# Optimization experiments

Hardware: AMD Instinct MI355X
Metric: run time of the kernel (lower is better)

## Reference

```python
import jax, jax.numpy as jnp
import numpy as np
from jax import lax

N = 100000
IN_C, HID, OUT_C = 512, 256, 128
K_STEPS = 10
ALPHA = 0.1
RES_ALPHA = 1.0
LN_EPS = 1e-5


def layer_norm(h, g, b):
    mu = jnp.mean(h, axis=-1, keepdims=True)
    var = jnp.mean(jnp.square(h - mu), axis=-1, keepdims=True)
    return (h - mu) * lax.rsqrt(var + LN_EPS) * g + b


def appnp(h, src, dst):
    # add self loops
    loop = jnp.arange(N, dtype=src.dtype)
    s = jnp.concatenate([src, loop])
    d = jnp.concatenate([dst, loop])
    ew = jnp.ones(s.shape[0], h.dtype)
    deg = jax.ops.segment_sum(ew, d, num_segments=N)
    dis = jnp.where(deg > 0, lax.rsqrt(jnp.maximum(deg, 1e-12)), 0.0)
    norm = dis[s] * ew * dis[d]  # [E+N]
    h0 = h
    def step(carry, _):
        msg = norm[:, None] * carry[s]                      # gather [E+N, C]
        agg = jax.ops.segment_sum(msg, d, num_segments=N)    # scatter-add
        return (1.0 - ALPHA) * agg + ALPHA * h0, None
    h, _ = lax.scan(step, h, None, length=K_STEPS)
    return h


def setup_inputs() -> dict:
    key = jax.random.key(0)
    ks = jax.random.split(key, 12)
    def lin(k, fan_in, fan_out):
        bound = 1.0 / np.sqrt(fan_in)
        kw, kb = jax.random.split(k)
        W = jax.random.uniform(kw, (fan_in, fan_out), jnp.float32, -bound, bound)
        b = jax.random.uniform(kb, (fan_out,), jnp.float32, -bound, bound)
        return W, b
    x = jax.random.normal(ks[0], (N, IN_C), jnp.float32)
    edge_index = jax.random.randint(ks[1], (2, 1600000), 0, N, jnp.int32)
    W_in, b_in = lin(ks[2], IN_C, HID)
    W1, b1 = lin(ks[3], HID, HID)
    W2, b2 = lin(ks[4], HID, HID)
    W_out, b_out = lin(ks[5], HID, OUT_C)
    g1 = jnp.ones(HID); be1 = jnp.zeros(HID)
    g2 = jnp.ones(HID); be2 = jnp.zeros(HID)
    return {"x": x, "edge_index": edge_index,
            "W_in": W_in, "b_in": b_in,
            "W1": W1, "b1": b1, "g1": g1, "be1": be1,
            "W2": W2, "b2": b2, "g2": g2, "be2": be2,
            "W_out": W_out, "b_out": b_out}


def reference(x, edge_index, W_in, b_in, W1, b1, g1, be1, W2, b2, g2, be2, W_out, b_out):
    # MLP with residual blocks (eval mode: no dropout)
    h = x @ W_in + b_in
    for (W, b, g, be) in ((W1, b1, g1, be1), (W2, b2, g2, be2)):
        identity = h
        h = layer_norm(h @ W + b, g, be)
        h = RES_ALPHA * h + (1.0 - RES_ALPHA) * identity
        h = jax.nn.relu(h)
    h = h @ W_out + b_out
    # APPNP propagation
    return appnp(h, edge_index[0], edge_index[1])
```

## Files before the change

kernel.cpp:

```cpp
#include <hip/hip_runtime.h>

typedef unsigned short u16;
typedef __attribute__((ext_vector_type(8))) short bfrag;
typedef __attribute__((ext_vector_type(4))) float f32x4;

__device__ inline float b2f(u16 u) {
    union { unsigned int i; float f; } v; v.i = ((unsigned int)u) << 16; return v.f;
}
__device__ inline u16 f2b(float f) {
    union { float f; unsigned int u; } v; v.f = f;
    unsigned int r = v.u + 0x7fffu + ((v.u >> 16) & 1u);
    return (u16)(r >> 16);
}
__device__ inline float ldF(const void* p, size_t i, bool bf) {
    return bf ? b2f(((const u16*)p)[i]) : ((const float*)p)[i];
}
__device__ inline void gload_lds16(const void* g, void* l) {
    __builtin_amdgcn_global_load_lds((const __attribute__((address_space(1))) unsigned int*)g,
                                     (__attribute__((address_space(3))) unsigned int*)l, 16, 0, 0);
}

__global__ void detect_k(const unsigned int* __restrict__ g1w, int* flag) {
    if (blockIdx.x == 0 && threadIdx.x == 0)
        *flag = (g1w[0] == 0x3F803F80u) ? 1 : 0;
}

__global__ void cvt_x(const void* __restrict__ in, u16* __restrict__ out, int n4,
                      const int* __restrict__ flagp) {
    int i = blockIdx.x * 256 + threadIdx.x;
    if (i >= n4) return;
    if (*flagp) {
        ((ushort4*)out)[i] = ((const ushort4*)in)[i];
    } else {
        const float4 v = ((const float4*)in)[i];
        ushort4 o; o.x = f2b(v.x); o.y = f2b(v.y); o.z = f2b(v.z); o.w = f2b(v.w);
        ((ushort4*)out)[i] = o;
    }
}

__global__ void cvt_h0b(const float* __restrict__ h0, u16* __restrict__ out, int n64) {
    int i = blockIdx.x * 256 + threadIdx.x;
    if (i >= n64) return;
    const float2 v = ((const float2*)h0)[i];
    ((unsigned int*)out)[i] = ((unsigned int)f2b(v.y) << 16) | (unsigned int)f2b(v.x);
}

__global__ void wt_k(const void* __restrict__ W, u16* __restrict__ Wt, int K, int NC,
                     const int* __restrict__ flagp) {
    int i = blockIdx.x * 256 + threadIdx.x;
    if (i >= K * NC) return;
    int k = i / NC, nn = i - k * NC;
    u16 v = (*flagp) ? ((const u16*)W)[i] : f2b(((const float*)W)[i]);
    Wt[(size_t)nn * K + k] = v;
}

template<int K, bool OUT_BF16>
__global__ __launch_bounds__(256) void gemm_bt(const u16* __restrict__ A, const u16* __restrict__ Bt,
                                               const void* __restrict__ bias, void* __restrict__ C,
                                               int M, int NC, const int* __restrict__ flagp) {
    const int BM = 128, BN = 128, BK = 32;
    __shared__ u16 As[2][BM * BK];
    __shared__ u16 Bs[2][BN * BK];
    const bool bf = (*flagp != 0);
    int nt = NC / BN;

    int nwg = gridDim.x, bid = blockIdx.x;
    int qc = nwg >> 3, rc = nwg & 7;
    int xcd = bid & 7, off = bid >> 3;
    int swz = (xcd < rc ? xcd * (qc + 1) : rc * (qc + 1) + (xcd - rc) * qc) + off;
    int m0 = (swz / nt) * BM;
    int n0 = (swz % nt) * BN;

    int t = threadIdx.x;
    int lane = t & 63, wave = t >> 6;
    int wm = (wave >> 1) * 64, wn = (wave & 1) * 64;

    f32x4 acc[4][4];
#pragma unroll
    for (int i = 0; i < 4; i++)
#pragma unroll
        for (int j = 0; j < 4; j++) acc[i][j] = (f32x4){0.f, 0.f, 0.f, 0.f};

    auto stage = [&](int bufi, int kk) {
#pragma unroll
        for (int q = 0; q < 2; ++q) {
            int idx = q * 256 + t;
            int row = idx >> 2;
            int cb  = (idx & 3) * 16;
            int ra = m0 + row; ra = ra < M ? ra : M - 1;
            const char* ga = (const char*)A  + ((size_t)ra * K) * 2 + kk * 2 + cb;
            const char* gb = (const char*)Bt + ((size_t)(n0 + row) * K) * 2 + kk * 2 + cb;
            char* la = (char*)&As[bufi][0] + q * 4096 + wave * 1024;
            char* lb = (char*)&Bs[bufi][0] + q * 4096 + wave * 1024;
            gload_lds16(ga, la);
            gload_lds16(gb, lb);
        }
    };

    stage(0, 0);
    __syncthreads();
    int cur = 0;
    int r16 = lane & 15, q8 = (lane >> 4) * 8;
    for (int k0 = 0; k0 < K; k0 += BK) {
        if (k0 + BK < K) stage(cur ^ 1, k0 + BK);
        bfrag a[4], b[4];
#pragma unroll
        for (int i = 0; i < 4; i++) a[i] = *(const bfrag*)&As[cur][(wm + i * 16 + r16) * BK + q8];
#pragma unroll
        for (int j = 0; j < 4; j++) b[j] = *(const bfrag*)&Bs[cur][(wn + j * 16 + r16) * BK + q8];
#pragma unroll
        for (int i = 0; i < 4; i++)
#pragma unroll
            for (int j = 0; j < 4; j++)
                acc[i][j] = __builtin_amdgcn_mfma_f32_16x16x32_bf16(a[i], b[j], acc[i][j], 0, 0, 0);
        __syncthreads();
        cur ^= 1;
    }

    int q4 = (lane >> 4) * 4;
#pragma unroll
    for (int j = 0; j < 4; j++) {
        int cg = n0 + wn + j * 16 + r16;
        float bvv = ldF(bias, cg, bf);
#pragma unroll
        for (int i = 0; i < 4; i++) {
#pragma unroll
            for (int rr = 0; rr < 4; rr++) {
                int rg = m0 + wm + i * 16 + q4 + rr;
                if (rg < M) {
                    float v = acc[i][j][rr] + bvv;
                    if (OUT_BF16) ((u16*)C)[(size_t)rg * NC + cg] = f2b(v);
                    else          ((float*)C)[(size_t)rg * NC + cg] = v;
                }
            }
        }
    }
}

__global__ __launch_bounds__(256) void ln_relu_k(const float* __restrict__ T, const void* __restrict__ g,
                                                 const void* __restrict__ be, u16* __restrict__ out,
                                                 int M, const int* __restrict__ flagp) {
    const bool bf = (*flagp != 0);
    int wave = threadIdx.x >> 6, lane = threadIdx.x & 63;
    int row = blockIdx.x * 4 + wave;
    if (row >= M) return;
    const float4 x = *(const float4*)(T + (size_t)row * 256 + lane * 4);
    float s = x.x + x.y + x.z + x.w;
    for (int o = 32; o > 0; o >>= 1) s += __shfl_xor(s, o);
    float mu = s * (1.0f / 256.0f);
    float d0 = x.x - mu, d1 = x.y - mu, d2 = x.z - mu, d3 = x.w - mu;
    float q = d0 * d0 + d1 * d1 + d2 * d2 + d3 * d3;
    for (int o = 32; o > 0; o >>= 1) q += __shfl_xor(q, o);
    float rs = rsqrtf(q * (1.0f / 256.0f) + 1e-5f);
    int c0 = lane * 4;
    float y0 = fmaxf(d0 * rs * ldF(g, c0 + 0, bf) + ldF(be, c0 + 0, bf), 0.f);
    float y1 = fmaxf(d1 * rs * ldF(g, c0 + 1, bf) + ldF(be, c0 + 1, bf), 0.f);
    float y2 = fmaxf(d2 * rs * ldF(g, c0 + 2, bf) + ldF(be, c0 + 2, bf), 0.f);
    float y3 = fmaxf(d3 * rs * ldF(g, c0 + 3, bf) + ldF(be, c0 + 3, bf), 0.f);
    ushort4 o4; o4.x = f2b(y0); o4.y = f2b(y1); o4.z = f2b(y2); o4.w = f2b(y3);
    *(ushort4*)(out + (size_t)row * 256 + c0) = o4;
}

__global__ void deg_init(int* deg, int n) {
    int i = blockIdx.x * 256 + threadIdx.x;
    if (i < n) deg[i] = 1;
}
__global__ void deg_count(const int* __restrict__ dst, int* deg, int E) {
    int i = blockIdx.x * 256 + threadIdx.x;
    if (i < E) atomicAdd(&deg[dst[i]], 1);
}
__global__ void dis_k(const int* __restrict__ deg, float* dis, int n) {
    int i = blockIdx.x * 256 + threadIdx.x;
    if (i < n) dis[i] = rsqrtf((float)deg[i]);
}

__global__ void scan_block(const int* __restrict__ deg, int* rowptr, int* bsum, int n) {
    __shared__ int sh[256];
    int t = threadIdx.x, i = blockIdx.x * 256 + t;
    int v = (i < n) ? deg[i] : 0;
    sh[t] = v; __syncthreads();
    for (int o = 1; o < 256; o <<= 1) {
        int x = (t >= o) ? sh[t - o] : 0;
        __syncthreads();
        sh[t] += x;
        __syncthreads();
    }
    if (i < n) rowptr[i] = sh[t] - v;
    if (t == 255) bsum[blockIdx.x] = sh[t];
}
__global__ void scan_sums(int* bsum, int nb) {
    __shared__ int sh[512];
    int t = threadIdx.x;
    int v = (t < nb) ? bsum[t] : 0;
    sh[t] = v; __syncthreads();
    for (int o = 1; o < 512; o <<= 1) {
        int x = (t >= o) ? sh[t - o] : 0;
        __syncthreads();
        sh[t] += x;
        __syncthreads();
    }
    if (t < nb) bsum[t] = sh[t] - v;
}
__global__ void scan_add(int* rowptr, const int* __restrict__ bsum, int n, int total) {
    int i = blockIdx.x * 256 + threadIdx.x;
    if (i < n) rowptr[i] += bsum[blockIdx.x];
    if (i == 0) rowptr[n] = total;
}
__global__ void fill_k(const int* __restrict__ src, const int* __restrict__ dst,
                       const int* __restrict__ rowptr, int* cursor, const float* __restrict__ dis,
                       int* col, float* wt, int E, int n) {
    int i = blockIdx.x * 256 + threadIdx.x;
    if (i >= E + n) return;
    int s, d;
    if (i < E) { s = src[i]; d = dst[i]; }
    else       { s = d = i - E; }
    int p = rowptr[d] + atomicAdd(&cursor[d], 1);
    col[p] = s;
    wt[p] = dis[s] * dis[d];
}

__global__ __launch_bounds__(256) void prop_k(const u16* __restrict__ curb, const float* __restrict__ h0,
                                              const int* __restrict__ rowptr, const int* __restrict__ col,
                                              const float* __restrict__ wt,
                                              u16* __restrict__ outB, void* __restrict__ outD,
                                              const int* __restrict__ flagp, int n) {
    int wave = threadIdx.x >> 6, lane = threadIdx.x & 63;
    int node = blockIdx.x * 4 + wave;
    if (node >= n) return;
    int p0 = rowptr[node], p1 = rowptr[node + 1];
    float ax = 0.f, ay = 0.f;
    for (int p = p0; p < p1; p += 64) {
        int cnt = p1 - p; if (cnt > 64) cnt = 64;
        int sj = 0; float wj = 0.f;
        if (lane < cnt) { sj = col[p + lane]; wj = wt[p + lane]; }
        for (int j = 0; j < cnt; j += 8) {
            float ww[8]; unsigned int v[8];
#pragma unroll
            for (int u = 0; u < 8; ++u) {
                int jj = j + u;
                bool ok = jj < cnt;
                if (!ok) jj = cnt - 1;
                int ss = __shfl(sj, jj);
                float w = __shfl(wj, jj);
                ww[u] = ok ? w : 0.f;
                v[u] = *(const unsigned int*)(curb + (size_t)ss * 128 + 2 * lane);
            }
#pragma unroll
            for (int u = 0; u < 8; ++u) {
                ax = fmaf(ww[u], b2f((u16)(v[u] & 0xffffu)), ax);
                ay = fmaf(ww[u], b2f((u16)(v[u] >> 16)), ay);
            }
        }
    }
    const float2 h = *(const float2*)(h0 + (size_t)node * 128 + 2 * lane);
    float rx = 0.9f * ax + 0.1f * h.x;
    float ry = 0.9f * ay + 0.1f * h.y;
    if (outB) {
        unsigned int pk = ((unsigned int)f2b(ry) << 16) | (unsigned int)f2b(rx);
        ((unsigned int*)outB)[(size_t)node * 64 + lane] = pk;
    } else if (*flagp) {
        unsigned int pk = ((unsigned int)f2b(ry) << 16) | (unsigned int)f2b(rx);
        ((unsigned int*)outD)[(size_t)node * 64 + lane] = pk;
    } else {
        float2 o; o.x = rx; o.y = ry;
        *(float2*)((float*)outD + (size_t)node * 128 + 2 * lane) = o;
    }
}

extern "C" void kernel_launch(void* const* d_in, const int* in_sizes, int n_in,
                              void* d_out, int out_size, void* d_ws, size_t ws_size,
                              hipStream_t stream) {
    const int N = in_sizes[0] / 512;
    const int E = in_sizes[1] / 2;
    const void* x    = d_in[0];
    const int*  ei   = (const int*)d_in[1];
    const void* Win  = d_in[2];
    const void* bin  = d_in[3];
    const void* W1   = d_in[4];
    const void* b1   = d_in[5];
    const void* g1   = d_in[6];
    const void* be1  = d_in[7];
    const void* W2   = d_in[8];
    const void* b2   = d_in[9];
    const void* g2   = d_in[10];
    const void* be2  = d_in[11];
    const void* Wout = d_in[12];
    const void* bout = d_in[13];
    (void)n_in; (void)out_size; (void)ws_size;

    char* w = (char*)d_ws;
    auto alloc = [&](size_t b) { char* p = w; w += (b + 255) & ~(size_t)255; return p; };
    char*  buf0 = alloc((size_t)N * 512 * 2);
    char*  actAraw = alloc((size_t)N * 256 * 2);
    float* h0   = (float*)alloc((size_t)N * 128 * 4);
    u16* WtIn  = (u16*)alloc((size_t)512 * 256 * 2);
    u16* Wt1   = (u16*)alloc((size_t)256 * 256 * 2);
    u16* Wt2   = (u16*)alloc((size_t)256 * 256 * 2);
    u16* WtOut = (u16*)alloc((size_t)256 * 128 * 2);
    int*   deg    = (int*)alloc((size_t)N * 4);
    float* dis    = (float*)alloc((size_t)N * 4);
    int*   rowptr = (int*)alloc((size_t)(N + 1) * 4);
    int*   cursor = (int*)alloc((size_t)N * 4);
    int*   bsum   = (int*)alloc(512 * 4);
    int*   flag   = (int*)alloc(256);
    u16*   xbf = (u16*)buf0;
    float* T   = (float*)buf0;
    u16*   h0b = (u16*)buf0;
    u16*   cA  = (u16*)(buf0 + (size_t)N * 128 * 2);
    u16*   cB  = (u16*)(buf0 + (size_t)N * 128 * 4);
    u16*   actA = (u16*)actAraw;
    int*   ecol = (int*)actAraw;
    float* ewt  = (float*)(actAraw + (size_t)(E + N) * 4);

    detect_k<<<1, 64, 0, stream>>>((const unsigned int*)g1, flag);

    int n4 = N * 512 / 4;
    cvt_x<<<(n4 + 255) / 256, 256, 0, stream>>>(x, xbf, n4, flag);
    wt_k<<<(512 * 256 + 255) / 256, 256, 0, stream>>>(Win,  WtIn,  512, 256, flag);
    wt_k<<<(256 * 256 + 255) / 256, 256, 0, stream>>>(W1,   Wt1,   256, 256, flag);
    wt_k<<<(256 * 256 + 255) / 256, 256, 0, stream>>>(W2,   Wt2,   256, 256, flag);
    wt_k<<<(256 * 128 + 255) / 256, 256, 0, stream>>>(Wout, WtOut, 256, 128, flag);

    int mt = (N + 127) / 128;
    gemm_bt<512, true ><<<mt * 2, 256, 0, stream>>>(xbf,  WtIn,  bin,  actA, N, 256, flag);
    gemm_bt<256, false><<<mt * 2, 256, 0, stream>>>(actA, Wt1,   b1,   T,    N, 256, flag);
    ln_relu_k<<<(N + 3) / 4, 256, 0, stream>>>(T, g1, be1, actA, N, flag);
    gemm_bt<256, false><<<mt * 2, 256, 0, stream>>>(actA, Wt2,   b2,   T,    N, 256, flag);
    ln_relu_k<<<(N + 3) / 4, 256, 0, stream>>>(T, g2, be2, actA, N, flag);
    gemm_bt<256, false><<<mt * 1, 256, 0, stream>>>(actA, WtOut, bout, h0,   N, 128, flag);

    cvt_h0b<<<(N * 64 + 255) / 256, 256, 0, stream>>>(h0, h0b, N * 64);

    deg_init <<<(N + 255) / 256, 256, 0, stream>>>(deg, N);
    deg_count<<<(E + 255) / 256, 256, 0, stream>>>(ei + E, deg, E);
    dis_k    <<<(N + 255) / 256, 256, 0, stream>>>(deg, dis, N);
    int nb = (N + 255) / 256;
    scan_block<<<nb, 256, 0, stream>>>(deg, rowptr, bsum, N);
    scan_sums<<<1, 512, 0, stream>>>(bsum, nb);
    scan_add<<<nb, 256, 0, stream>>>(rowptr, bsum, N, E + N);
    hipMemsetAsync(cursor, 0, (size_t)N * 4, stream);
    fill_k<<<(E + N + 255) / 256, 256, 0, stream>>>(ei, ei + E, rowptr, cursor, dis, ecol, ewt, E, N);

    const u16* cur = h0b;
    for (int it = 0; it < 10; ++it) {
        bool last = (it == 9);
        u16* o = (it & 1) ? cB : cA;
        prop_k<<<(N + 3) / 4, 256, 0, stream>>>(cur, h0, rowptr, ecol, ewt,
                                                last ? nullptr : o,
                                                last ? d_out : nullptr, flag, N);
        cur = o;
    }
}
```

Baseline: 1.520 ms.

## Pack edge col/weight, store h0 in bf16, unroll gather by sixteen

Edge source index and weight are packed into one int2 array, so each edge costs one load instead of two. The output GEMM now writes h0 directly in bf16, which removes the fp32 h0 buffer and the separate conversion kernel, and each propagation step reads the bf16 copy for its residual term. The gather inner loop is unrolled to 16 outstanding loads to raise memory-level parallelism, and the degree init kernel is replaced by a memset with the self-loop +1 folded into later kernels. The bf16 residual adds rounding error to the alpha*h0 term, and the wider unroll raises register use.

```diff
diff --git a/kernel.cpp b/kernel.cpp
--- a/kernel.cpp
+++ b/kernel.cpp
@@ -36,13 +36,6 @@
         ushort4 o; o.x = f2b(v.x); o.y = f2b(v.y); o.z = f2b(v.z); o.w = f2b(v.w);
         ((ushort4*)out)[i] = o;
     }
-}
-
-__global__ void cvt_h0b(const float* __restrict__ h0, u16* __restrict__ out, int n64) {
-    int i = blockIdx.x * 256 + threadIdx.x;
-    if (i >= n64) return;
-    const float2 v = ((const float2*)h0)[i];
-    ((unsigned int*)out)[i] = ((unsigned int)f2b(v.y) << 16) | (unsigned int)f2b(v.x);
 }
 
 __global__ void wt_k(const void* __restrict__ W, u16* __restrict__ Wt, int K, int NC,
@@ -161,23 +154,19 @@
     *(ushort4*)(out + (size_t)row * 256 + c0) = o4;
 }
 
-__global__ void deg_init(int* deg, int n) {
-    int i = blockIdx.x * 256 + threadIdx.x;
-    if (i < n) deg[i] = 1;
-}
 __global__ void deg_count(const int* __restrict__ dst, int* deg, int E) {
     int i = blockIdx.x * 256 + threadIdx.x;
     if (i < E) atomicAdd(&deg[dst[i]], 1);
 }
 __global__ void dis_k(const int* __restrict__ deg, float* dis, int n) {
     int i = blockIdx.x * 256 + threadIdx.x;
-    if (i < n) dis[i] = rsqrtf((float)deg[i]);
+    if (i < n) dis[i] = rsqrtf((float)(deg[i] + 1));
 }
 
 __global__ void scan_block(const int* __restrict__ deg, int* rowptr, int* bsum, int n) {
     __shared__ int sh[256];
     int t = threadIdx.x, i = blockIdx.x * 256 + t;
-    int v = (i < n) ? deg[i] : 0;
+    int v = (i < n) ? deg[i] + 1 : 0;
     sh[t] = v; __syncthreads();
     for (int o = 1; o < 256; o <<= 1) {
         int x = (t >= o) ? sh[t - o] : 0;
@@ -208,20 +197,20 @@
 }
 __global__ void fill_k(const int* __restrict__ src, const int* __restrict__ dst,
                        const int* __restrict__ rowptr, int* cursor, const float* __restrict__ dis,
-                       int* col, float* wt, int E, int n) {
+                       int2* __restrict__ epack, int E, int n) {
     int i = blockIdx.x * 256 + threadIdx.x;
     if (i >= E + n) return;
     int s, d;
     if (i < E) { s = src[i]; d = dst[i]; }
     else       { s = d = i - E; }
     int p = rowptr[d] + atomicAdd(&cursor[d], 1);
-    col[p] = s;
-    wt[p] = dis[s] * dis[d];
-}
-
-__global__ __launch_bounds__(256) void prop_k(const u16* __restrict__ curb, const float* __restrict__ h0,
-                                              const int* __restrict__ rowptr, const int* __restrict__ col,
-                                              const float* __restrict__ wt,
+    float wv = dis[s] * dis[d];
+    int2 e; e.x = s; e.y = __float_as_int(wv);
+    epack[p] = e;
+}
+
+__global__ __launch_bounds__(256) void prop_k(const u16* __restrict__ curb, const u16* __restrict__ h0b,
+                                              const int* __restrict__ rowptr, const int2* __restrict__ epack,
                                               u16* __restrict__ outB, void* __restrict__ outD,
                                               const int* __restrict__ flagp, int n) {
     int wave = threadIdx.x >> 6, lane = threadIdx.x & 63;
@@ -232,11 +221,14 @@
     for (int p = p0; p < p1; p += 64) {
         int cnt = p1 - p; if (cnt > 64) cnt = 64;
         int sj = 0; float wj = 0.f;
-        if (lane < cnt) { sj = col[p + lane]; wj = wt[p + lane]; }
-        for (int j = 0; j < cnt; j += 8) {
-            float ww[8]; unsigned int v[8];
-#pragma unroll
-            for (int u = 0; u < 8; ++u) {
+        if (lane < cnt) {
+            int2 e = epack[p + lane];
+            sj = e.x; wj = __int_as_float(e.y);
+        }
+        for (int j = 0; j < cnt; j += 16) {
+            float ww[16]; unsigned int v[16];
+#pragma unroll
+            for (int u = 0; u < 16; ++u) {
                 int jj = j + u;
                 bool ok = jj < cnt;
                 if (!ok) jj = cnt - 1;
@@ -246,15 +238,15 @@
                 v[u] = *(const unsigned int*)(curb + (size_t)ss * 128 + 2 * lane);
             }
 #pragma unroll
-            for (int u = 0; u < 8; ++u) {
+            for (int u = 0; u < 16; ++u) {
                 ax = fmaf(ww[u], b2f((u16)(v[u] & 0xffffu)), ax);
                 ay = fmaf(ww[u], b2f((u16)(v[u] >> 16)), ay);
             }
         }
     }
-    const float2 h = *(const float2*)(h0 + (size_t)node * 128 + 2 * lane);
-    float rx = 0.9f * ax + 0.1f * h.x;
-    float ry = 0.9f * ay + 0.1f * h.y;
+    unsigned int hp = ((const unsigned int*)h0b)[(size_t)node * 64 + lane];
+    float rx = 0.9f * ax + 0.1f * b2f((u16)(hp & 0xffffu));
+    float ry = 0.9f * ay + 0.1f * b2f((u16)(hp >> 16));
     if (outB) {
         unsigned int pk = ((unsigned int)f2b(ry) << 16) | (unsigned int)f2b(rx);
         ((unsigned int*)outB)[(size_t)node * 64 + lane] = pk;
@@ -292,7 +284,6 @@
     auto alloc = [&](size_t b) { char* p = w; w += (b + 255) & ~(size_t)255; return p; };
     char*  buf0 = alloc((size_t)N * 512 * 2);
     char*  actAraw = alloc((size_t)N * 256 * 2);
-    float* h0   = (float*)alloc((size_t)N * 128 * 4);
     u16* WtIn  = (u16*)alloc((size_t)512 * 256 * 2);
     u16* Wt1   = (u16*)alloc((size_t)256 * 256 * 2);
     u16* Wt2   = (u16*)alloc((size_t)256 * 256 * 2);
@@ -308,9 +299,8 @@
     u16*   h0b = (u16*)buf0;
     u16*   cA  = (u16*)(buf0 + (size_t)N * 128 * 2);
     u16*   cB  = (u16*)(buf0 + (size_t)N * 128 * 4);
-    u16*   actA = (u16*)actAraw;
-    int*   ecol = (int*)actAraw;
-    float* ewt  = (float*)(actAraw + (size_t)(E + N) * 4);
+    u16*   actA  = (u16*)actAraw;
+    int2*  epack = (int2*)actAraw;
 
     detect_k<<<1, 64, 0, stream>>>((const unsigned int*)g1, flag);
 
@@ -327,11 +317,9 @@
     ln_relu_k<<<(N + 3) / 4, 256, 0, stream>>>(T, g1, be1, actA, N, flag);
     gemm_bt<256, false><<<mt * 2, 256, 0, stream>>>(actA, Wt2,   b2,   T,    N, 256, flag);
     ln_relu_k<<<(N + 3) / 4, 256, 0, stream>>>(T, g2, be2, actA, N, flag);
-    gemm_bt<256, false><<<mt * 1, 256, 0, stream>>>(actA, WtOut, bout, h0,   N, 128, flag);
-
-    cvt_h0b<<<(N * 64 + 255) / 256, 256, 0, stream>>>(h0, h0b, N * 64);
-
-    deg_init <<<(N + 255) / 256, 256, 0, stream>>>(deg, N);
+    gemm_bt<256, true ><<<mt * 1, 256, 0, stream>>>(actA, WtOut, bout, h0b,  N, 128, flag);
+
+    hipMemsetAsync(deg, 0, (size_t)N * 4, stream);
     deg_count<<<(E + 255) / 256, 256, 0, stream>>>(ei + E, deg, E);
     dis_k    <<<(N + 255) / 256, 256, 0, stream>>>(deg, dis, N);
     int nb = (N + 255) / 256;
@@ -339,13 +327,13 @@
     scan_sums<<<1, 512, 0, stream>>>(bsum, nb);
     scan_add<<<nb, 256, 0, stream>>>(rowptr, bsum, N, E + N);
     hipMemsetAsync(cursor, 0, (size_t)N * 4, stream);
-    fill_k<<<(E + N + 255) / 256, 256, 0, stream>>>(ei, ei + E, rowptr, cursor, dis, ecol, ewt, E, N);
+    fill_k<<<(E + N + 255) / 256, 256, 0, stream>>>(ei, ei + E, rowptr, cursor, dis, epack, E, N);
 
     const u16* cur = h0b;
     for (int it = 0; it < 10; ++it) {
         bool last = (it == 9);
         u16* o = (it & 1) ? cB : cA;
-        prop_k<<<(N + 3) / 4, 256, 0, stream>>>(cur, h0, rowptr, ecol, ewt,
+        prop_k<<<(N + 3) / 4, 256, 0, stream>>>(cur, h0b, rowptr, epack,
                                                 last ? nullptr : o,
                                                 last ? d_out : nullptr, flag, N);
         cur = o;
```

Result: faster. 1.463 ms (-3.8%).
